# Kernel tuning notes

Measured on AMD Instinct MI355X. Metric: run time of the kernel, lower is better.

Reference implementation:

```python
import jax, jax.numpy as jnp
import numpy as np

GRID_SIZE = 5
SPLINE_ORDER = 3
LN_EPS = 1e-5


def make_grid(dtype=jnp.float32):
    # efficient-kan default grid over [-1, 1], extended by spline_order on each side
    h = 2.0 / GRID_SIZE
    return jnp.arange(-SPLINE_ORDER, GRID_SIZE + SPLINE_ORDER + 1, dtype=dtype) * h - 1.0  # (12,)


def b_splines(x, grid):
    # Cox-de Boor recursion. x: (B, Cin) -> bases: (B, Cin, GRID_SIZE+SPLINE_ORDER)
    xe = x[..., None]  # (B, Cin, 1)
    bases = ((xe >= grid[:-1]) & (xe < grid[1:])).astype(x.dtype)  # order-0, (B,Cin,11)
    for k in range(1, SPLINE_ORDER + 1):
        left = (xe - grid[: -(k + 1)]) / (grid[k:-1] - grid[: -(k + 1)]) * bases[..., :-1]
        right = (grid[k + 1:] - xe) / (grid[k + 1:] - grid[1:-k]) * bases[..., 1:]
        bases = left + right
    return bases


def setup_inputs() -> dict:
    key = jax.random.key(0)
    k0, k1, k2, k3 = jax.random.split(key, 4)
    B, T, C, O = 512, 197, 768, 1000
    G = GRID_SIZE + SPLINE_ORDER
    x = jax.random.normal(k0, (B, T, C), jnp.float32)
    ln_weight = jnp.ones((T, C), jnp.float32)
    ln_bias = jnp.zeros((T, C), jnp.float32)
    base_weight = jax.random.normal(k1, (O, C), jnp.float32) * (1.0 / np.sqrt(C))
    spline_weight = jax.random.normal(k2, (O, C, G), jnp.float32) * 0.1
    spline_scaler = 1.0 + 0.1 * jax.random.normal(k3, (O, C), jnp.float32)
    return {"x": x, "ln_weight": ln_weight, "ln_bias": ln_bias,
            "base_weight": base_weight, "spline_weight": spline_weight,
            "spline_scaler": spline_scaler}


def reference(x, ln_weight, ln_bias, base_weight, spline_weight, spline_scaler):
    # LayerNorm over the last two dims [n_tokens, n_channel]
    mean = x.mean(axis=(1, 2), keepdims=True)
    var = x.var(axis=(1, 2), keepdims=True)  # biased, as in torch LayerNorm
    xn = (x - mean) * jax.lax.rsqrt(var + LN_EPS) * ln_weight + ln_bias
    # permute -> AdaptiveAvgPool1d(1) -> squeeze == mean over token axis
    pooled = xn.mean(axis=1)  # (B, C)
    # KANLinear: base path (SiLU + linear) + spline path
    base_out = jax.nn.silu(pooled) @ base_weight.T  # (B, O)
    grid = make_grid(pooled.dtype)
    splines = b_splines(pooled, grid)  # (B, C, 8)
    scaled_w = spline_weight * spline_scaler[..., None]  # (O, C, 8)
    spline_out = jnp.einsum('bcg,ocg->bo', splines, scaled_w)
    return base_out + spline_out
```

## Files before the change

kernel.cpp:

```cpp
#include <hip/hip_runtime.h>
#include <hip/hip_bf16.h>
#include <cstdint>

#define B_SZ 512
#define T_SZ 197
#define C_SZ 768
#define O_SZ 1000
#define K_SZ (C_SZ + C_SZ * 8)
#define NPAD 1024
#define LN_EPS 1e-5f

typedef __bf16 bf16;
typedef __bf16 bf16x4 __attribute__((ext_vector_type(4)));
typedef __bf16 bf16x8 __attribute__((ext_vector_type(8)));
typedef float  f32x4  __attribute__((ext_vector_type(4)));

__global__ __launch_bounds__(256) void k0_wbmean(
    const float* __restrict__ lnw, const float* __restrict__ lnb,
    float* __restrict__ wmean, float* __restrict__ bmean)
{
    const int tid  = threadIdx.x;
    const int cl   = tid & 31;
    const int c    = blockIdx.x * 32 + cl;
    const int tsub = tid >> 5;
    float sw = 0.f, sb = 0.f;
    for (int t = tsub; t < T_SZ; t += 8) {
        sw += lnw[t * C_SZ + c];
        sb += lnb[t * C_SZ + c];
    }
    __shared__ float rs[8][32], rb[8][32];
    rs[tsub][cl] = sw;
    rb[tsub][cl] = sb;
    __syncthreads();
    if (tsub == 0) {
        float SW = 0.f, SB = 0.f;
        #pragma unroll
        for (int i = 0; i < 8; ++i) { SW += rs[i][cl]; SB += rb[i][cl]; }
        const float invT = 1.0f / T_SZ;
        wmean[c] = SW * invT;
        bmean[c] = SB * invT;
    }
}

__global__ __launch_bounds__(256) void kz_zero(float4* __restrict__ out)
{
    out[blockIdx.x * 256 + threadIdx.x] = make_float4(0.f, 0.f, 0.f, 0.f);
}

__global__ __launch_bounds__(256) void k2_prep_w(
    const float* __restrict__ bw, const float* __restrict__ sw,
    const float* __restrict__ ss, bf16* __restrict__ Wc)
{
    const int o = blockIdx.x;
    const int tid = threadIdx.x;
    bf16* row = Wc + (size_t)o * K_SZ;
    if (o >= O_SZ) {
        bf16x8 z = {};
        for (int i = tid; i < K_SZ / 8; i += 256)
            *(bf16x8*)(row + i * 8) = z;
        return;
    }
    for (int c = tid; c < C_SZ; c += 256)
        row[c] = (bf16)bw[(size_t)o * C_SZ + c];
    for (int c = tid; c < C_SZ; c += 256) {
        float sc = ss[(size_t)o * C_SZ + c];
        const float4* swp = (const float4*)(sw + ((size_t)o * C_SZ + c) * 8);
        float4 w0 = swp[0], w1 = swp[1];
        bf16x8 v;
        v[0] = (bf16)(w0.x * sc); v[1] = (bf16)(w0.y * sc);
        v[2] = (bf16)(w0.z * sc); v[3] = (bf16)(w0.w * sc);
        v[4] = (bf16)(w1.x * sc); v[5] = (bf16)(w1.y * sc);
        v[6] = (bf16)(w1.z * sc); v[7] = (bf16)(w1.w * sc);
        *(bf16x8*)(row + C_SZ + (size_t)c * 8) = v;
    }
}

__global__ __launch_bounds__(384) void k1_pool_feat(
    const float* __restrict__ x, const float* __restrict__ lnw,
    const float* __restrict__ wmean, const float* __restrict__ bmean,
    bf16* __restrict__ Act)
{
    const int b   = blockIdx.x;
    const int tid = threadIdx.x;
    const int u   = tid % 192;
    const int rg  = tid / 192;

    const float4* X4 = (const float4*)(x + (size_t)b * T_SZ * C_SZ);
    const float4* W4 = (const float4*)lnw;

    float4 a4 = make_float4(0.f, 0.f, 0.f, 0.f);
    float s = 0.f, s2 = 0.f;
    for (int r = rg; r < T_SZ; r += 2) {
        float4 xv = X4[r * 192 + u];
        float4 wv = W4[r * 192 + u];
        a4.x += wv.x * xv.x; a4.y += wv.y * xv.y;
        a4.z += wv.z * xv.z; a4.w += wv.w * xv.w;
        s  += xv.x + xv.y + xv.z + xv.w;
        s2 += xv.x * xv.x + xv.y * xv.y + xv.z * xv.z + xv.w * xv.w;
    }
    for (int off = 32; off > 0; off >>= 1) {
        s  += __shfl_down(s,  off, 64);
        s2 += __shfl_down(s2, off, 64);
    }
    __shared__ float red_s[6], red_s2[6];
    __shared__ float4 aShare[192];
    __shared__ float stats[2];
    const int wave = tid >> 6, lane = tid & 63;
    if (lane == 0) { red_s[wave] = s; red_s2[wave] = s2; }
    if (rg == 1) aShare[u] = a4;
    __syncthreads();
    if (tid == 0) {
        float S = 0.f, S2 = 0.f;
        for (int i = 0; i < 6; ++i) { S += red_s[i]; S2 += red_s2[i]; }
        const float invN = 1.0f / (float)(T_SZ * C_SZ);
        float mean = S * invN;
        float var  = S2 * invN - mean * mean;
        stats[0] = mean;
        stats[1] = rsqrtf(var + LN_EPS);
    }
    __syncthreads();
    if (rg == 0) {
        const float mean = stats[0], rstd = stats[1];
        float4 ao = aShare[u];
        a4.x += ao.x; a4.y += ao.y; a4.z += ao.z; a4.w += ao.w;
        const float invT = 1.0f / T_SZ;
        float p[4];
        bf16x4 basev;
        const float av[4] = { a4.x, a4.y, a4.z, a4.w };
        #pragma unroll
        for (int j = 0; j < 4; ++j) {
            int c = 4 * u + j;
            float pv = rstd * (av[j] * invT - mean * wmean[c]) + bmean[c];
            p[j] = pv;
            float si = pv / (1.f + expf(-pv));
            basev[j] = (bf16)si;
        }
        *(bf16x4*)(Act + (size_t)b * K_SZ + 4 * u) = basev;
        #pragma unroll
        for (int j = 0; j < 4; ++j) {
            float pv = p[j];
            float bas[11];
            #pragma unroll
            for (int i = 0; i < 11; ++i) {
                float g0 = (i - 3) * 0.4f - 1.0f;
                float g1 = (i - 2) * 0.4f - 1.0f;
                bas[i] = (pv >= g0 && pv < g1) ? 1.0f : 0.0f;
            }
            #pragma unroll
            for (int k = 1; k <= 3; ++k) {
                #pragma unroll
                for (int i = 0; i + k < 11; ++i) {
                    float gi   = (i - 3) * 0.4f - 1.0f;
                    float gik  = (i + k - 3) * 0.4f - 1.0f;
                    float gik1 = (i + k - 2) * 0.4f - 1.0f;
                    float gi1  = (i - 2) * 0.4f - 1.0f;
                    float left  = (pv - gi) / (gik - gi) * bas[i];
                    float right = (gik1 - pv) / (gik1 - gi1) * bas[i + 1];
                    bas[i] = left + right;
                }
            }
            bf16x8 sv;
            #pragma unroll
            for (int g = 0; g < 8; ++g) sv[g] = (bf16)bas[g];
            *(bf16x8*)(Act + (size_t)b * K_SZ + C_SZ + (size_t)(4 * u + j) * 8) = sv;
        }
    }
}

__global__ __launch_bounds__(256) void k3_gemm(
    const bf16* __restrict__ Act, const bf16* __restrict__ Wc,
    float* __restrict__ Out)
{
    __shared__ __align__(16) bf16 As[64][72];
    __shared__ __align__(16) bf16 Bs[64][72];
    const int tid  = threadIdx.x;
    const int tile = blockIdx.x & 127;
    const int ks   = blockIdx.x >> 7;
    const int bm   = tile & 7;
    const int bn   = tile >> 3;
    const int m0   = bm * 64, n0 = bn * 64;
    const int kbeg = ks * (K_SZ / 2), kend = kbeg + K_SZ / 2;
    const int wave = tid >> 6, lane = tid & 63;
    const int wr   = (wave >> 1) * 32, wc = (wave & 1) * 32;
    const int lr   = lane & 15, lk = (lane >> 4) * 8;

    f32x4 acc[2][2] = {};
    const int r0 = tid >> 3,          c0 = (tid & 7) * 8;
    const int r1 = (256 + tid) >> 3,  c1 = c0;

    for (int k0 = kbeg; k0 < kend; k0 += 64) {
        uint4 a0 = *(const uint4*)(Act + (size_t)(m0 + r0) * K_SZ + k0 + c0);
        uint4 a1 = *(const uint4*)(Act + (size_t)(m0 + r1) * K_SZ + k0 + c1);
        uint4 b0 = *(const uint4*)(Wc  + (size_t)(n0 + r0) * K_SZ + k0 + c0);
        uint4 b1 = *(const uint4*)(Wc  + (size_t)(n0 + r1) * K_SZ + k0 + c1);
        *(uint4*)(&As[r0][c0]) = a0;
        *(uint4*)(&As[r1][c1]) = a1;
        *(uint4*)(&Bs[r0][c0]) = b0;
        *(uint4*)(&Bs[r1][c1]) = b1;
        __syncthreads();
        #pragma unroll
        for (int kk = 0; kk < 64; kk += 32) {
            bf16x8 af[2], bfr[2];
            #pragma unroll
            for (int mi = 0; mi < 2; ++mi)
                af[mi] = *(const bf16x8*)(&As[wr + mi * 16 + lr][kk + lk]);
            #pragma unroll
            for (int ni = 0; ni < 2; ++ni)
                bfr[ni] = *(const bf16x8*)(&Bs[wc + ni * 16 + lr][kk + lk]);
            #pragma unroll
            for (int mi = 0; mi < 2; ++mi)
                #pragma unroll
                for (int ni = 0; ni < 2; ++ni)
                    acc[mi][ni] = __builtin_amdgcn_mfma_f32_16x16x32_bf16(
                        af[mi], bfr[ni], acc[mi][ni], 0, 0, 0);
        }
        __syncthreads();
    }
    #pragma unroll
    for (int mi = 0; mi < 2; ++mi)
        #pragma unroll
        for (int ni = 0; ni < 2; ++ni) {
            int col = n0 + wc + ni * 16 + lr;
            if (col < O_SZ) {
                #pragma unroll
                for (int j = 0; j < 4; ++j) {
                    int rowi = m0 + wr + mi * 16 + (lane >> 4) * 4 + j;
                    unsafeAtomicAdd(&Out[(size_t)rowi * O_SZ + col], acc[mi][ni][j]);
                }
            }
        }
}

extern "C" void kernel_launch(void* const* d_in, const int* in_sizes, int n_in,
                              void* d_out, int out_size, void* d_ws, size_t ws_size,
                              hipStream_t stream)
{
    const float* x   = (const float*)d_in[0];
    const float* lnw = (const float*)d_in[1];
    const float* lnb = (const float*)d_in[2];
    const float* bw  = (const float*)d_in[3];
    const float* sw  = (const float*)d_in[4];
    const float* ss  = (const float*)d_in[5];
    float* Out = (float*)d_out;

    char* ws = (char*)d_ws;
    float* wmean = (float*)ws;
    float* bmean = wmean + C_SZ;
    bf16*  Act   = (bf16*)(ws + 8192);
    bf16*  Wcat  = (bf16*)(ws + 8192 + (size_t)B_SZ * K_SZ * 2);

    k0_wbmean<<<24, 256, 0, stream>>>(lnw, lnb, wmean, bmean);
    kz_zero<<<500, 256, 0, stream>>>((float4*)Out);
    k2_prep_w<<<NPAD, 256, 0, stream>>>(bw, sw, ss, Wcat);
    k1_pool_feat<<<B_SZ, 384, 0, stream>>>(x, lnw, wmean, bmean, Act);
    k3_gemm<<<256, 256, 0, stream>>>(Act, Wcat, Out);
}
```

Before: 524.1 us.

## Double-buffer GEMM with direct global-to-LDS loads, 4-way split-K, wider pooling blocks

```diff
diff --git a/kernel.cpp b/kernel.cpp
--- a/kernel.cpp
+++ b/kernel.cpp
@@ -15,36 +15,41 @@
 typedef __bf16 bf16x8 __attribute__((ext_vector_type(8)));
 typedef float  f32x4  __attribute__((ext_vector_type(4)));
 
-__global__ __launch_bounds__(256) void k0_wbmean(
+__device__ __forceinline__ void gload_lds16(const void* g, void* l) {
+    __builtin_amdgcn_global_load_lds(
+        (const __attribute__((address_space(1))) unsigned int*)g,
+        (__attribute__((address_space(3))) unsigned int*)l, 16, 0, 0);
+}
+
+__global__ __launch_bounds__(256) void k0_wbz(
     const float* __restrict__ lnw, const float* __restrict__ lnb,
-    float* __restrict__ wmean, float* __restrict__ bmean)
-{
-    const int tid  = threadIdx.x;
-    const int cl   = tid & 31;
-    const int c    = blockIdx.x * 32 + cl;
-    const int tsub = tid >> 5;
-    float sw = 0.f, sb = 0.f;
-    for (int t = tsub; t < T_SZ; t += 8) {
-        sw += lnw[t * C_SZ + c];
-        sb += lnb[t * C_SZ + c];
-    }
-    __shared__ float rs[8][32], rb[8][32];
-    rs[tsub][cl] = sw;
-    rb[tsub][cl] = sb;
-    __syncthreads();
-    if (tsub == 0) {
-        float SW = 0.f, SB = 0.f;
-        #pragma unroll
-        for (int i = 0; i < 8; ++i) { SW += rs[i][cl]; SB += rb[i][cl]; }
-        const float invT = 1.0f / T_SZ;
-        wmean[c] = SW * invT;
-        bmean[c] = SB * invT;
-    }
-}
-
-__global__ __launch_bounds__(256) void kz_zero(float4* __restrict__ out)
-{
-    out[blockIdx.x * 256 + threadIdx.x] = make_float4(0.f, 0.f, 0.f, 0.f);
+    float* __restrict__ wmean, float* __restrict__ bmean,
+    float4* __restrict__ out)
+{
+    const int tid = threadIdx.x;
+    out[blockIdx.x * 256 + tid] = make_float4(0.f, 0.f, 0.f, 0.f);
+    if (blockIdx.x < 24) {
+        const int cl   = tid & 31;
+        const int c    = blockIdx.x * 32 + cl;
+        const int tsub = tid >> 5;
+        float sw = 0.f, sb = 0.f;
+        for (int t = tsub; t < T_SZ; t += 8) {
+            sw += lnw[t * C_SZ + c];
+            sb += lnb[t * C_SZ + c];
+        }
+        __shared__ float rs[8][32], rb[8][32];
+        rs[tsub][cl] = sw;
+        rb[tsub][cl] = sb;
+        __syncthreads();
+        if (tsub == 0) {
+            float SW = 0.f, SB = 0.f;
+            #pragma unroll
+            for (int i = 0; i < 8; ++i) { SW += rs[i][cl]; SB += rb[i][cl]; }
+            const float invT = 1.0f / T_SZ;
+            wmean[c] = SW * invT;
+            bmean[c] = SB * invT;
+        }
+    }
 }
 
 __global__ __launch_bounds__(256) void k2_prep_w(
@@ -75,7 +80,7 @@
     }
 }
 
-__global__ __launch_bounds__(384) void k1_pool_feat(
+__global__ __launch_bounds__(768) void k1_pool_feat(
     const float* __restrict__ x, const float* __restrict__ lnw,
     const float* __restrict__ wmean, const float* __restrict__ bmean,
     bf16* __restrict__ Act)
@@ -90,7 +95,7 @@
 
     float4 a4 = make_float4(0.f, 0.f, 0.f, 0.f);
     float s = 0.f, s2 = 0.f;
-    for (int r = rg; r < T_SZ; r += 2) {
+    for (int r = rg; r < T_SZ; r += 4) {
         float4 xv = X4[r * 192 + u];
         float4 wv = W4[r * 192 + u];
         a4.x += wv.x * xv.x; a4.y += wv.y * xv.y;
@@ -102,16 +107,16 @@
         s  += __shfl_down(s,  off, 64);
         s2 += __shfl_down(s2, off, 64);
     }
-    __shared__ float red_s[6], red_s2[6];
-    __shared__ float4 aShare[192];
+    __shared__ float red_s[12], red_s2[12];
+    __shared__ float4 aShare[3][192];
     __shared__ float stats[2];
     const int wave = tid >> 6, lane = tid & 63;
     if (lane == 0) { red_s[wave] = s; red_s2[wave] = s2; }
-    if (rg == 1) aShare[u] = a4;
+    if (rg >= 1) aShare[rg - 1][u] = a4;
     __syncthreads();
     if (tid == 0) {
         float S = 0.f, S2 = 0.f;
-        for (int i = 0; i < 6; ++i) { S += red_s[i]; S2 += red_s2[i]; }
+        for (int i = 0; i < 12; ++i) { S += red_s[i]; S2 += red_s2[i]; }
         const float invN = 1.0f / (float)(T_SZ * C_SZ);
         float mean = S * invN;
         float var  = S2 * invN - mean * mean;
@@ -121,8 +126,11 @@
     __syncthreads();
     if (rg == 0) {
         const float mean = stats[0], rstd = stats[1];
-        float4 ao = aShare[u];
-        a4.x += ao.x; a4.y += ao.y; a4.z += ao.z; a4.w += ao.w;
+        #pragma unroll
+        for (int g = 0; g < 3; ++g) {
+            float4 ao = aShare[g][u];
+            a4.x += ao.x; a4.y += ao.y; a4.z += ao.z; a4.w += ao.w;
+        }
         const float invT = 1.0f / T_SZ;
         float p[4];
         bf16x4 basev;
@@ -171,42 +179,55 @@
     const bf16* __restrict__ Act, const bf16* __restrict__ Wc,
     float* __restrict__ Out)
 {
-    __shared__ __align__(16) bf16 As[64][72];
-    __shared__ __align__(16) bf16 Bs[64][72];
+    __shared__ __align__(16) char lds[2][16384];
     const int tid  = threadIdx.x;
     const int tile = blockIdx.x & 127;
     const int ks   = blockIdx.x >> 7;
     const int bm   = tile & 7;
     const int bn   = tile >> 3;
     const int m0   = bm * 64, n0 = bn * 64;
-    const int kbeg = ks * (K_SZ / 2), kend = kbeg + K_SZ / 2;
+    const int kbeg = ks * (K_SZ / 4), kend = kbeg + K_SZ / 4;
     const int wave = tid >> 6, lane = tid & 63;
     const int wr   = (wave >> 1) * 32, wc = (wave & 1) * 32;
-    const int lr   = lane & 15, lk = (lane >> 4) * 8;
+    const int lr   = lane & 15, lq = lane >> 4;
+
+    const int srow = tid >> 3;
+    const int scol = (((tid & 7) ^ (srow & 7)) << 3);
+    const size_t aoff = (size_t)(m0 + srow) * K_SZ + scol;
+    const size_t boff = (size_t)(n0 + srow) * K_SZ + scol;
+    char* const lwb = lds[0] + (wave << 10);
 
     f32x4 acc[2][2] = {};
-    const int r0 = tid >> 3,          c0 = (tid & 7) * 8;
-    const int r1 = (256 + tid) >> 3,  c1 = c0;
-
+
+    #define STAGE(buf, kk0)  do {                                              \
+        char* lb_ = lwb + (buf) * 16384;                                       \
+        gload_lds16(Act + aoff + (kk0), lb_);                                  \
+        gload_lds16(Act + aoff + (size_t)32 * K_SZ + (kk0), lb_ + 4096);       \
+        gload_lds16(Wc  + boff + (kk0), lb_ + 8192);                           \
+        gload_lds16(Wc  + boff + (size_t)32 * K_SZ + (kk0), lb_ + 12288);      \
+    } while (0)
+
+    STAGE(0, kbeg);
+    __syncthreads();
+    int cur = 0;
     for (int k0 = kbeg; k0 < kend; k0 += 64) {
-        uint4 a0 = *(const uint4*)(Act + (size_t)(m0 + r0) * K_SZ + k0 + c0);
-        uint4 a1 = *(const uint4*)(Act + (size_t)(m0 + r1) * K_SZ + k0 + c1);
-        uint4 b0 = *(const uint4*)(Wc  + (size_t)(n0 + r0) * K_SZ + k0 + c0);
-        uint4 b1 = *(const uint4*)(Wc  + (size_t)(n0 + r1) * K_SZ + k0 + c1);
-        *(uint4*)(&As[r0][c0]) = a0;
-        *(uint4*)(&As[r1][c1]) = a1;
-        *(uint4*)(&Bs[r0][c0]) = b0;
-        *(uint4*)(&Bs[r1][c1]) = b1;
-        __syncthreads();
+        if (k0 + 64 < kend) STAGE(cur ^ 1, k0 + 64);
+        const char* la = lds[cur];
+        const char* lbm = lds[cur] + 8192;
         #pragma unroll
         for (int kk = 0; kk < 64; kk += 32) {
+            const int sbase = (kk >> 3) + lq;
             bf16x8 af[2], bfr[2];
             #pragma unroll
-            for (int mi = 0; mi < 2; ++mi)
-                af[mi] = *(const bf16x8*)(&As[wr + mi * 16 + lr][kk + lk]);
-            #pragma unroll
-            for (int ni = 0; ni < 2; ++ni)
-                bfr[ni] = *(const bf16x8*)(&Bs[wc + ni * 16 + lr][kk + lk]);
+            for (int mi = 0; mi < 2; ++mi) {
+                int row = wr + mi * 16 + lr;
+                af[mi] = *(const bf16x8*)(la + row * 128 + ((sbase ^ (row & 7)) << 4));
+            }
+            #pragma unroll
+            for (int ni = 0; ni < 2; ++ni) {
+                int row = wc + ni * 16 + lr;
+                bfr[ni] = *(const bf16x8*)(lbm + row * 128 + ((sbase ^ (row & 7)) << 4));
+            }
             #pragma unroll
             for (int mi = 0; mi < 2; ++mi)
                 #pragma unroll
@@ -215,7 +236,10 @@
                         af[mi], bfr[ni], acc[mi][ni], 0, 0, 0);
         }
         __syncthreads();
-    }
+        cur ^= 1;
+    }
+    #undef STAGE
+
     #pragma unroll
     for (int mi = 0; mi < 2; ++mi)
         #pragma unroll
@@ -224,7 +248,7 @@
             if (col < O_SZ) {
                 #pragma unroll
                 for (int j = 0; j < 4; ++j) {
-                    int rowi = m0 + wr + mi * 16 + (lane >> 4) * 4 + j;
+                    int rowi = m0 + wr + mi * 16 + lq * 4 + j;
                     unsafeAtomicAdd(&Out[(size_t)rowi * O_SZ + col], acc[mi][ni][j]);
                 }
             }
@@ -249,9 +273,8 @@
     bf16*  Act   = (bf16*)(ws + 8192);
     bf16*  Wcat  = (bf16*)(ws + 8192 + (size_t)B_SZ * K_SZ * 2);
 
-    k0_wbmean<<<24, 256, 0, stream>>>(lnw, lnb, wmean, bmean);
-    kz_zero<<<500, 256, 0, stream>>>((float4*)Out);
+    k0_wbz<<<500, 256, 0, stream>>>(lnw, lnb, wmean, bmean, (float4*)Out);
     k2_prep_w<<<NPAD, 256, 0, stream>>>(bw, sw, ss, Wcat);
-    k1_pool_feat<<<B_SZ, 384, 0, stream>>>(x, lnw, wmean, bmean, Act);
-    k3_gemm<<<256, 256, 0, stream>>>(Act, Wcat, Out);
-}
+    k1_pool_feat<<<B_SZ, 768, 0, stream>>>(x, lnw, wmean, bmean, Act);
+    k3_gemm<<<512, 256, 0, stream>>>(Act, Wcat, Out);
+}
```

New measurement: 495.7 us. 5.4% less time.
